# Optimization experiments

Hardware: AMD Instinct MI355X
Metric: run time of the kernel (lower is better)

Reference implementation:

```python
import jax, jax.numpy as jnp
import numpy as np

N_NODES = 100000
N_EDGES = 1250000
HID = 64
IN_CH = 64
OUT_CH = 16
N_GRAPHS = 512


def setup_inputs() -> dict:
    key = jax.random.key(0)
    ks = jax.random.split(key, 20)
    x = jax.random.normal(ks[0], (N_NODES, IN_CH), dtype=jnp.float32)
    edge_index = jax.random.randint(ks[1], (2, N_EDGES), 0, N_NODES, dtype=jnp.int64)
    batch = jnp.sort(jax.random.randint(ks[2], (N_NODES,), 0, N_GRAPHS, dtype=jnp.int64))
    s_in = 1.0 / np.sqrt(IN_CH)
    s_h = 1.0 / np.sqrt(HID)
    u = lambda k, shp, s: jax.random.uniform(k, shp, jnp.float32, -s, s)
    return {
        "x": x, "edge_index": edge_index, "batch": batch,
        "W0": u(ks[3], (IN_CH, HID), s_in), "b0": u(ks[4], (HID,), s_in),
        "W1a": u(ks[5], (HID, HID), s_h), "b1a": u(ks[6], (HID,), s_h),
        "W1b": u(ks[7], (HID, HID), s_h), "b1b": u(ks[8], (HID,), s_h),
        "W2a": u(ks[9], (HID, HID), s_h), "b2a": u(ks[10], (HID,), s_h),
        "W2b": u(ks[11], (HID, HID), s_h), "b2b": u(ks[12], (HID,), s_h),
        "W3a": u(ks[13], (HID, HID), s_h), "b3a": u(ks[14], (HID,), s_h),
        "W3b": u(ks[15], (HID, HID), s_h), "b3b": u(ks[16], (HID,), s_h),
        "Wl": u(ks[17], (HID, OUT_CH), s_h), "bl": u(ks[18], (OUT_CH,), s_h),
    }


def _gin_conv(h, src, dst, Wa, ba, Wb, bb):
    # GINConv, eps=0: mlp(x_i + sum_{j->i} x_j); mlp = Linear,ReLU,Linear
    agg = jax.ops.segment_sum(h[src], dst, num_segments=N_NODES)  # [N, HID]
    z = h + agg
    return jax.nn.relu(z @ Wa + ba) @ Wb + bb


def reference(x, edge_index, batch, W0, b0, W1a, b1a, W1b, b1b,
              W2a, b2a, W2b, b2b, W3a, b3a, W3b, b3b, Wl, bl):
    src, dst = edge_index[0], edge_index[1]
    h = jax.nn.relu(x @ W0 + b0)
    h = jax.nn.relu(_gin_conv(h, src, dst, W1a, b1a, W1b, b1b))
    h = jax.nn.relu(_gin_conv(h, src, dst, W2a, b2a, W2b, b2b))
    h = jax.nn.relu(_gin_conv(h, src, dst, W3a, b3a, W3b, b3b))
    # global mean pool over graphs
    sums = jax.ops.segment_sum(h, batch, num_segments=N_GRAPHS)  # [G, HID]
    cnts = jax.ops.segment_sum(jnp.ones((N_NODES,), h.dtype), batch, num_segments=N_GRAPHS)
    pooled = sums / jnp.maximum(cnts, 1.0)[:, None]
    # dropout p=0.5 is identity in eval mode
    return pooled @ Wl + bl  # [G, OUT_CH]
```

## Files before the change

kernel.cpp:

```cpp
#include <hip/hip_runtime.h>
#include <hip/hip_fp16.h>

#define N_NODES 100000
#define N_EDGES 1250000
#define HID 64
#define N_GRAPHS 512
#define OUT_CH 16

#define NSUP 196
#define SB_CAP 8192
#define E_BLK 2048
#define NPB ((N_EDGES + E_BLK - 1) / E_BLK)
#define TILE2 ((N_NODES + 127) / 128)
#define NWP 6
#define TSTRIDE 68
#define AGG_BLOCKS 3125
#define SMEM_UNION 37888

typedef _Float16 h16;
typedef _Float16 half2_t __attribute__((ext_vector_type(2)));
typedef _Float16 f16x8 __attribute__((ext_vector_type(8)));
typedef float f32x4 __attribute__((ext_vector_type(4)));

__device__ __forceinline__ void acc8(uint4 u, float* a) {
    half2_t h0 = __builtin_bit_cast(half2_t, u.x);
    half2_t h1 = __builtin_bit_cast(half2_t, u.y);
    half2_t h2 = __builtin_bit_cast(half2_t, u.z);
    half2_t h3 = __builtin_bit_cast(half2_t, u.w);
    a[0] += (float)h0[0]; a[1] += (float)h0[1];
    a[2] += (float)h1[0]; a[3] += (float)h1[1];
    a[4] += (float)h2[0]; a[5] += (float)h2[1];
    a[6] += (float)h3[0]; a[7] += (float)h3[1];
}

__device__ __forceinline__ unsigned pack2(float x, float y) {
    half2_t o;
    o[0] = (h16)x;
    o[1] = (h16)y;
    return __builtin_bit_cast(unsigned, o);
}

__global__ __launch_bounds__(256) void k_part(const int* __restrict__ src,
                                              const int* __restrict__ dst,
                                              int* __restrict__ cnt,
                                              int* __restrict__ buckets,
                                              const float* __restrict__ W1a,
                                              const float* __restrict__ W1b,
                                              const float* __restrict__ W2a,
                                              const float* __restrict__ W2b,
                                              const float* __restrict__ W3a,
                                              const float* __restrict__ W3b,
                                              h16* __restrict__ WF) {
    __shared__ int hist[256];
    __shared__ int gbase[256];
    __shared__ int tsum[256];
    __shared__ __align__(16) int stage[E_BLK];

    int b = blockIdx.x;
    int t = threadIdx.x;

    if (b < NPB) {
        int e0 = b * E_BLK;
        int eN = N_EDGES - e0;
        if (eN > E_BLK) eN = E_BLK;

        hist[t] = 0;
        __syncthreads();
        for (int i = t; i < eN; i += 256) atomicAdd(&hist[dst[e0 + i] >> 9], 1);
        __syncthreads();

        int c = hist[t];
        tsum[t] = c;
        __syncthreads();
        for (int off = 1; off < 256; off <<= 1) {
            int u = (t >= off) ? tsum[t - off] : 0;
            __syncthreads();
            tsum[t] += u;
            __syncthreads();
        }
        int pref = tsum[t] - c;
        if (t < NSUP && c > 0) gbase[t] = atomicAdd(&cnt[t], c);
        hist[t] = pref;
        __syncthreads();

        for (int i = t; i < eN; i += 256) {
            int s = src[e0 + i];
            int d = dst[e0 + i];
            int p = atomicAdd(&hist[d >> 9], 1);
            stage[p] = ((d & 511) << 17) | s;
        }
        __syncthreads();

        if (t < NSUP && c > 0) {
            int lstart = hist[t] - c;
            int gb = gbase[t];
            int cap = SB_CAP - gb;
            int n = c < cap ? c : (cap > 0 ? cap : 0);
            int* dp = buckets + (size_t)t * SB_CAP + gb;
            int r = 0;
            while (r < n && (((size_t)(dp + r)) & 15)) { dp[r] = stage[lstart + r]; ++r; }
            for (; r + 4 <= n; r += 4) {
                int4 v;
                v.x = stage[lstart + r];
                v.y = stage[lstart + r + 1];
                v.z = stage[lstart + r + 2];
                v.w = stage[lstart + r + 3];
                *(int4*)(dp + r) = v;
            }
            for (; r < n; ++r) dp[r] = stage[lstart + r];
        }
    } else {
        const float* Ws[NWP] = {W1a, W1b, W2a, W2b, W3a, W3b};
        const float* W = Ws[b - NPB];
        h16* dstW = WF + (size_t)(b - NPB) * 4096;
#pragma unroll
        for (int i = 0; i < 16; ++i) {
            int s = t + 256 * i;
            int k = s >> 6, col = s & 63;
            int kc = k >> 5, quad = (k >> 3) & 3, j = k & 7;
            int c = col >> 4, n = col & 15;
            dstW[((c * 2 + kc) * 4 + quad) * 128 + n * 8 + j] = (h16)W[s];
        }
    }
}

__global__ __launch_bounds__(256) void k_sortlin(const int* __restrict__ cnt,
                                                 int* __restrict__ buckets,
                                                 int* __restrict__ rowptrS,
                                                 const float* __restrict__ W0,
                                                 const float* __restrict__ B0,
                                                 const float* __restrict__ Xin,
                                                 h16* __restrict__ Hout) {
    __shared__ __align__(16) char smem[SMEM_UNION];
    int b = blockIdx.x;
    int t = threadIdx.x;

    if (b < NSUP) {
        int* srt  = (int*)smem;
        int* hist = (int*)(smem + 32768);
        int* curs = (int*)(smem + 34816);
        int* tsum = (int*)(smem + 36864);
        int s = b;
        int n = cnt[s];
        n = n < SB_CAP ? n : SB_CAP;
        int* gb = buckets + (size_t)s * SB_CAP;
        int sBase = s * SB_CAP;

        hist[t] = 0;
        hist[t + 256] = 0;
        __syncthreads();
        for (int i = t; i < n; i += 256) atomicAdd(&hist[gb[i] >> 17], 1);
        __syncthreads();

        int c0 = hist[2 * t], c1 = hist[2 * t + 1];
        int tot = c0 + c1;
        tsum[t] = tot;
        __syncthreads();
        for (int off = 1; off < 256; off <<= 1) {
            int u = (t >= off) ? tsum[t - off] : 0;
            __syncthreads();
            tsum[t] += u;
            __syncthreads();
        }
        int pref = tsum[t] - tot;
        curs[2 * t] = pref;
        curs[2 * t + 1] = pref + c0;
        rowptrS[s * 513 + 2 * t] = sBase + pref;
        rowptrS[s * 513 + 2 * t + 1] = sBase + pref + c0;
        if (t == 255) rowptrS[s * 513 + 512] = sBase + n;
        __syncthreads();

        for (int i = t; i < n; i += 256) {
            int rec = gb[i];
            int pos = atomicAdd(&curs[rec >> 17], 1);
            srt[pos] = rec;
        }
        __syncthreads();
        for (int i = t; i < n; i += 256) gb[i] = srt[i];
    } else {
        float* sT = (float*)smem;
        int lb = b - NSUP;
        int w = t >> 6, lane = t & 63;
        int n16 = lane & 15, quad = lane >> 4;
        float* T = sT + w * 16 * TSTRIDE;

        f16x8 bw[4][2];
#pragma unroll
        for (int c = 0; c < 4; ++c)
#pragma unroll
            for (int kc = 0; kc < 2; ++kc) {
                f16x8 v;
#pragma unroll
                for (int j = 0; j < 8; ++j)
                    v[j] = (h16)W0[(kc * 32 + quad * 8 + j) * 64 + c * 16 + n16];
                bw[c][kc] = v;
            }
        float bv[4];
#pragma unroll
        for (int c = 0; c < 4; ++c) bv[c] = B0[c * 16 + n16];

#pragma unroll
        for (int tt = 0; tt < 2; ++tt) {
            int rbase = lb * 128 + tt * 64 + w * 16;
            int arow = rbase + n16;
            int crow = arow < N_NODES ? arow : N_NODES - 1;
            f16x8 a[2];
#pragma unroll
            for (int kc = 0; kc < 2; ++kc) {
                const float4* xp = (const float4*)(Xin + (size_t)crow * HID + kc * 32 + quad * 8);
                float4 p = xp[0], q = xp[1];
                f16x8 v;
                v[0] = (h16)p.x; v[1] = (h16)p.y; v[2] = (h16)p.z; v[3] = (h16)p.w;
                v[4] = (h16)q.x; v[5] = (h16)q.y; v[6] = (h16)q.z; v[7] = (h16)q.w;
                a[kc] = v;
            }

            f32x4 acc[4];
#pragma unroll
            for (int c = 0; c < 4; ++c) {
                acc[c] = (f32x4){bv[c], bv[c], bv[c], bv[c]};
#pragma unroll
                for (int kc = 0; kc < 2; ++kc)
                    acc[c] = __builtin_amdgcn_mfma_f32_16x16x32_f16(a[kc], bw[c][kc], acc[c], 0, 0, 0);
            }

#pragma unroll
            for (int c = 0; c < 4; ++c)
#pragma unroll
                for (int r = 0; r < 4; ++r)
                    T[(quad * 4 + r) * TSTRIDE + c * 16 + n16] = fmaxf(acc[c][r], 0.f);
            {
                int rl = lane >> 2, seg = lane & 3;
                int row = rbase + rl;
                if (row < N_NODES) {
                    const float* tr = &T[rl * TSTRIDE + seg * 16];
                    f16x8 o0, o1;
#pragma unroll
                    for (int i = 0; i < 8; ++i) {
                        o0[i] = (h16)tr[i];
                        o1[i] = (h16)tr[8 + i];
                    }
                    f16x8* dp = (f16x8*)(Hout + (size_t)row * HID + seg * 16);
                    dp[0] = o0;
                    dp[1] = o1;
                }
            }
            __syncthreads();
        }
    }
}

__global__ __launch_bounds__(256) void k_aggregate(const int* __restrict__ rowptrS,
                                                   const int* __restrict__ buckets,
                                                   const h16* __restrict__ H,
                                                   h16* __restrict__ Z) {
    const uint4* H8 = (const uint4*)H;
    uint4* Z8 = (uint4*)Z;
    int lane = threadIdx.x & 63;
    int part = lane >> 3, sub = lane & 7;
    int gwave = (blockIdx.x * 256 + threadIdx.x) >> 6;
    int nw = (gridDim.x * 256) >> 6;
    for (int i0 = gwave * 8; i0 < N_NODES; i0 += nw * 8) {
        int i = i0 + part;
        bool valid = i < N_NODES;
        int iv = valid ? i : N_NODES - 1;
        int s = iv >> 9, l = iv & 511;
        int start = rowptrS[s * 513 + l];
        int end = valid ? rowptrS[s * 513 + l + 1] : start;
        float a[8] = {0.f, 0.f, 0.f, 0.f, 0.f, 0.f, 0.f, 0.f};
        acc8(H8[(size_t)iv * 8 + sub], a);
        int deg = end - start;
        if (deg > 0) {
            int last = end - 1;
            int ix[16];
#pragma unroll
            for (int k = 0; k < 16; ++k) {
                int p = start + k;
                ix[k] = buckets[p < last ? p : last] & 0x1FFFF;
            }
            uint4 u[8];
#pragma unroll
            for (int k = 0; k < 8; ++k)
                if (deg > k) u[k] = H8[(size_t)ix[k] * 8 + sub];
#pragma unroll
            for (int k = 0; k < 8; ++k)
                if (deg > k) acc8(u[k], a);
            if (deg > 8) {
#pragma unroll
                for (int k = 0; k < 8; ++k)
                    if (deg > 8 + k) u[k] = H8[(size_t)ix[8 + k] * 8 + sub];
#pragma unroll
                for (int k = 0; k < 8; ++k)
                    if (deg > 8 + k) acc8(u[k], a);
            }
            if (deg > 16) {
                int j = start + 16;
                for (; j + 8 <= end; j += 8) {
                    int s0 = buckets[j] & 0x1FFFF;
                    int s1 = buckets[j + 1] & 0x1FFFF;
                    int s2 = buckets[j + 2] & 0x1FFFF;
                    int s3 = buckets[j + 3] & 0x1FFFF;
                    int s4 = buckets[j + 4] & 0x1FFFF;
                    int s5 = buckets[j + 5] & 0x1FFFF;
                    int s6 = buckets[j + 6] & 0x1FFFF;
                    int s7 = buckets[j + 7] & 0x1FFFF;
                    uint4 v0 = H8[(size_t)s0 * 8 + sub];
                    uint4 v1 = H8[(size_t)s1 * 8 + sub];
                    uint4 v2 = H8[(size_t)s2 * 8 + sub];
                    uint4 v3 = H8[(size_t)s3 * 8 + sub];
                    uint4 v4 = H8[(size_t)s4 * 8 + sub];
                    uint4 v5 = H8[(size_t)s5 * 8 + sub];
                    uint4 v6 = H8[(size_t)s6 * 8 + sub];
                    uint4 v7 = H8[(size_t)s7 * 8 + sub];
                    acc8(v0, a); acc8(v1, a); acc8(v2, a); acc8(v3, a);
                    acc8(v4, a); acc8(v5, a); acc8(v6, a); acc8(v7, a);
                }
                if (j + 4 <= end) {
                    int s0 = buckets[j] & 0x1FFFF;
                    int s1 = buckets[j + 1] & 0x1FFFF;
                    int s2 = buckets[j + 2] & 0x1FFFF;
                    int s3 = buckets[j + 3] & 0x1FFFF;
                    uint4 v0 = H8[(size_t)s0 * 8 + sub];
                    uint4 v1 = H8[(size_t)s1 * 8 + sub];
                    uint4 v2 = H8[(size_t)s2 * 8 + sub];
                    uint4 v3 = H8[(size_t)s3 * 8 + sub];
                    acc8(v0, a); acc8(v1, a); acc8(v2, a); acc8(v3, a);
                    j += 4;
                }
                if (j + 2 <= end) {
                    int s0 = buckets[j] & 0x1FFFF;
                    int s1 = buckets[j + 1] & 0x1FFFF;
                    uint4 v0 = H8[(size_t)s0 * 8 + sub];
                    uint4 v1 = H8[(size_t)s1 * 8 + sub];
                    acc8(v0, a); acc8(v1, a);
                    j += 2;
                }
                if (j < end) {
                    int s0 = buckets[j] & 0x1FFFF;
                    acc8(H8[(size_t)s0 * 8 + sub], a);
                }
            }
        }
        if (valid) {
            uint4 o;
            o.x = pack2(a[0], a[1]);
            o.y = pack2(a[2], a[3]);
            o.z = pack2(a[4], a[5]);
            o.w = pack2(a[6], a[7]);
            Z8[(size_t)i * 8 + sub] = o;
        }
    }
}

__global__ __launch_bounds__(256) void k_mlp(const h16* __restrict__ WaF,
                                             const float* __restrict__ Ba,
                                             const h16* __restrict__ WbF,
                                             const float* __restrict__ Bb,
                                             const h16* __restrict__ Zin,
                                             h16* __restrict__ Hout) {
    __shared__ __align__(16) float sT[4 * 16 * TSTRIDE];
    int t = threadIdx.x;
    int w = t >> 6, lane = t & 63;
    int n16 = lane & 15, quad = lane >> 4;
    float* T = sT + w * 16 * TSTRIDE;

    f16x8 bwa[4][2], bwb[4][2];
#pragma unroll
    for (int c = 0; c < 4; ++c)
#pragma unroll
        for (int kc = 0; kc < 2; ++kc) {
            int f = ((c * 2 + kc) * 4 + quad) * 128 + n16 * 8;
            bwa[c][kc] = *(const f16x8*)(WaF + f);
            bwb[c][kc] = *(const f16x8*)(WbF + f);
        }
    float bva[4], bvb[4];
#pragma unroll
    for (int c = 0; c < 4; ++c) {
        bva[c] = Ba[c * 16 + n16];
        bvb[c] = Bb[c * 16 + n16];
    }

#pragma unroll
    for (int tt = 0; tt < 2; ++tt) {
        int rbase = blockIdx.x * 128 + tt * 64 + w * 16;
        int arow = rbase + n16;
        int crow = arow < N_NODES ? arow : N_NODES - 1;
        const f16x8* zp = (const f16x8*)(Zin + (size_t)crow * HID + quad * 8);
        f16x8 a0 = zp[0];
        f16x8 a1 = zp[4];

        f32x4 acc[4];
#pragma unroll
        for (int c = 0; c < 4; ++c) {
            acc[c] = (f32x4){bva[c], bva[c], bva[c], bva[c]};
            acc[c] = __builtin_amdgcn_mfma_f32_16x16x32_f16(a0, bwa[c][0], acc[c], 0, 0, 0);
            acc[c] = __builtin_amdgcn_mfma_f32_16x16x32_f16(a1, bwa[c][1], acc[c], 0, 0, 0);
        }

#pragma unroll
        for (int c = 0; c < 4; ++c)
#pragma unroll
            for (int r = 0; r < 4; ++r)
                T[(quad * 4 + r) * TSTRIDE + c * 16 + n16] = fmaxf(acc[c][r], 0.f);

        f16x8 ta[2];
#pragma unroll
        for (int kc = 0; kc < 2; ++kc) {
            float4 p = *(const float4*)&T[n16 * TSTRIDE + kc * 32 + quad * 8];
            float4 q = *(const float4*)&T[n16 * TSTRIDE + kc * 32 + quad * 8 + 4];
            f16x8 v;
            v[0] = (h16)p.x; v[1] = (h16)p.y; v[2] = (h16)p.z; v[3] = (h16)p.w;
            v[4] = (h16)q.x; v[5] = (h16)q.y; v[6] = (h16)q.z; v[7] = (h16)q.w;
            ta[kc] = v;
        }

#pragma unroll
        for (int c = 0; c < 4; ++c) {
            acc[c] = (f32x4){bvb[c], bvb[c], bvb[c], bvb[c]};
            acc[c] = __builtin_amdgcn_mfma_f32_16x16x32_f16(ta[0], bwb[c][0], acc[c], 0, 0, 0);
            acc[c] = __builtin_amdgcn_mfma_f32_16x16x32_f16(ta[1], bwb[c][1], acc[c], 0, 0, 0);
        }

#pragma unroll
        for (int c = 0; c < 4; ++c)
#pragma unroll
            for (int r = 0; r < 4; ++r)
                T[(quad * 4 + r) * TSTRIDE + c * 16 + n16] = fmaxf(acc[c][r], 0.f);
        {
            int rl = lane >> 2, seg = lane & 3;
            int row = rbase + rl;
            if (row < N_NODES) {
                const float* tr = &T[rl * TSTRIDE + seg * 16];
                f16x8 o0, o1;
#pragma unroll
                for (int i = 0; i < 8; ++i) {
                    o0[i] = (h16)tr[i];
                    o1[i] = (h16)tr[8 + i];
                }
                f16x8* dp = (f16x8*)(Hout + (size_t)row * HID + seg * 16);
                dp[0] = o0;
                dp[1] = o1;
            }
        }
    }
}

__global__ __launch_bounds__(256) void k_poolfinal(const h16* __restrict__ H,
                                                   const int* __restrict__ batch,
                                                   const float* __restrict__ Wl,
                                                   const float* __restrict__ bl,
                                                   float* __restrict__ out) {
    __shared__ float sp[4 * HID];
    int g = blockIdx.x;
    int t = threadIdx.x;
    int lane = t & 63, w = t >> 6;
    int lo = 0, hi = N_NODES;
    while (lo < hi) { int m = (lo + hi) >> 1; if (batch[m] < g) lo = m + 1; else hi = m; }
    int start = lo;
    hi = N_NODES;
    while (lo < hi) { int m = (lo + hi) >> 1; if (batch[m] < g + 1) lo = m + 1; else hi = m; }
    int end = lo;
    float s0 = 0.f, s1 = 0.f, s2 = 0.f, s3 = 0.f;
    int r = start + w;
    for (; r + 12 < end; r += 16) {
        float v0 = (float)H[(size_t)r * HID + lane];
        float v1 = (float)H[(size_t)(r + 4) * HID + lane];
        float v2 = (float)H[(size_t)(r + 8) * HID + lane];
        float v3 = (float)H[(size_t)(r + 12) * HID + lane];
        s0 += v0; s1 += v1; s2 += v2; s3 += v3;
    }
    for (; r < end; r += 4) s0 += (float)H[(size_t)r * HID + lane];
    sp[w * HID + lane] = s0 + s1 + s2 + s3;
    __syncthreads();
    if (t < HID) {
        float tot = sp[t] + sp[HID + t] + sp[2 * HID + t] + sp[3 * HID + t];
        float c = (end > start) ? (float)(end - start) : 1.0f;
        sp[t] = tot / c;
    }
    __syncthreads();
    if (t < OUT_CH) {
        float acc = bl[t];
#pragma unroll
        for (int k = 0; k < HID; ++k) acc += sp[k] * Wl[k * OUT_CH + t];
        out[g * OUT_CH + t] = acc;
    }
}

extern "C" void kernel_launch(void* const* d_in, const int* in_sizes, int n_in,
                              void* d_out, int out_size, void* d_ws, size_t ws_size,
                              hipStream_t stream) {
    const float* x     = (const float*)d_in[0];
    const int*   edge  = (const int*)d_in[1];
    const int*   batch = (const int*)d_in[2];
    const float* W0  = (const float*)d_in[3];
    const float* b0  = (const float*)d_in[4];
    const float* W1a = (const float*)d_in[5];
    const float* b1a = (const float*)d_in[6];
    const float* W1b = (const float*)d_in[7];
    const float* b1b = (const float*)d_in[8];
    const float* W2a = (const float*)d_in[9];
    const float* b2a = (const float*)d_in[10];
    const float* W2b = (const float*)d_in[11];
    const float* b2b = (const float*)d_in[12];
    const float* W3a = (const float*)d_in[13];
    const float* b3a = (const float*)d_in[14];
    const float* W3b = (const float*)d_in[15];
    const float* b3b = (const float*)d_in[16];
    const float* Wl  = (const float*)d_in[17];
    const float* bl  = (const float*)d_in[18];
    float* out = (float*)d_out;

    const int* src = edge;
    const int* dst = edge + N_EDGES;

    h16* HA = (h16*)d_ws;
    h16* Z  = HA + (size_t)N_NODES * HID;
    int* cnt     = (int*)(Z + (size_t)N_NODES * HID);
    int* rowptrS = cnt + NSUP;
    int* buckets = rowptrS + NSUP * 513;
    h16* WF      = (h16*)(buckets + (size_t)NSUP * SB_CAP);
    h16* W1aF = WF;
    h16* W1bF = WF + 4096 * 1;
    h16* W2aF = WF + 4096 * 2;
    h16* W2bF = WF + 4096 * 3;
    h16* W3aF = WF + 4096 * 4;
    h16* W3bF = WF + 4096 * 5;

    hipMemsetAsync(cnt, 0, NSUP * sizeof(int), stream);
    k_part<<<NPB + NWP, 256, 0, stream>>>(src, dst, cnt, buckets,
        W1a, W1b, W2a, W2b, W3a, W3b, WF);
    k_sortlin<<<NSUP + TILE2, 256, 0, stream>>>(cnt, buckets, rowptrS, W0, b0, x, HA);

    k_aggregate<<<AGG_BLOCKS, 256, 0, stream>>>(rowptrS, buckets, HA, Z);
    k_mlp<<<TILE2, 256, 0, stream>>>(W1aF, b1a, W1bF, b1b, Z, HA);

    k_aggregate<<<AGG_BLOCKS, 256, 0, stream>>>(rowptrS, buckets, HA, Z);
    k_mlp<<<TILE2, 256, 0, stream>>>(W2aF, b2a, W2bF, b2b, Z, HA);

    k_aggregate<<<AGG_BLOCKS, 256, 0, stream>>>(rowptrS, buckets, HA, Z);
    k_mlp<<<TILE2, 256, 0, stream>>>(W3aF, b3a, W3bF, b3b, Z, HA);

    k_poolfinal<<<N_GRAPHS, 256, 0, stream>>>(HA, batch, Wl, bl, out);
}
```

Before: 274.8 us.

## Fuse final MLP with mean-pool accumulation and simplify aggregate gather loop

The last GIN MLP now accumulates its ReLU output directly into per-graph sums, using shared-memory slots plus global atomics, so the final H is never written or re-read. A small kernel then divides by the node counts and applies the output linear layer. The aggregate kernel's gather loop drops the prefetched 16-index front end and uses one plain unrolled-by-8 loop, which shrinks code and register use but may lose some early memory-level parallelism for low-degree nodes. The workspace layout is rearranged and the memset is widened to also zero the graph sums.

```diff
diff --git a/kernel.cpp b/kernel.cpp
--- a/kernel.cpp
+++ b/kernel.cpp
@@ -16,6 +16,7 @@
 #define TSTRIDE 68
 #define AGG_BLOCKS 3125
 #define SMEM_UNION 37888
+#define GP_SLOTS 16
 
 typedef _Float16 h16;
 typedef _Float16 half2_t __attribute__((ext_vector_type(2)));
@@ -269,77 +270,50 @@
         int end = valid ? rowptrS[s * 513 + l + 1] : start;
         float a[8] = {0.f, 0.f, 0.f, 0.f, 0.f, 0.f, 0.f, 0.f};
         acc8(H8[(size_t)iv * 8 + sub], a);
-        int deg = end - start;
-        if (deg > 0) {
-            int last = end - 1;
-            int ix[16];
-#pragma unroll
-            for (int k = 0; k < 16; ++k) {
-                int p = start + k;
-                ix[k] = buckets[p < last ? p : last] & 0x1FFFF;
-            }
-            uint4 u[8];
-#pragma unroll
-            for (int k = 0; k < 8; ++k)
-                if (deg > k) u[k] = H8[(size_t)ix[k] * 8 + sub];
-#pragma unroll
-            for (int k = 0; k < 8; ++k)
-                if (deg > k) acc8(u[k], a);
-            if (deg > 8) {
-#pragma unroll
-                for (int k = 0; k < 8; ++k)
-                    if (deg > 8 + k) u[k] = H8[(size_t)ix[8 + k] * 8 + sub];
-#pragma unroll
-                for (int k = 0; k < 8; ++k)
-                    if (deg > 8 + k) acc8(u[k], a);
-            }
-            if (deg > 16) {
-                int j = start + 16;
-                for (; j + 8 <= end; j += 8) {
-                    int s0 = buckets[j] & 0x1FFFF;
-                    int s1 = buckets[j + 1] & 0x1FFFF;
-                    int s2 = buckets[j + 2] & 0x1FFFF;
-                    int s3 = buckets[j + 3] & 0x1FFFF;
-                    int s4 = buckets[j + 4] & 0x1FFFF;
-                    int s5 = buckets[j + 5] & 0x1FFFF;
-                    int s6 = buckets[j + 6] & 0x1FFFF;
-                    int s7 = buckets[j + 7] & 0x1FFFF;
-                    uint4 v0 = H8[(size_t)s0 * 8 + sub];
-                    uint4 v1 = H8[(size_t)s1 * 8 + sub];
-                    uint4 v2 = H8[(size_t)s2 * 8 + sub];
-                    uint4 v3 = H8[(size_t)s3 * 8 + sub];
-                    uint4 v4 = H8[(size_t)s4 * 8 + sub];
-                    uint4 v5 = H8[(size_t)s5 * 8 + sub];
-                    uint4 v6 = H8[(size_t)s6 * 8 + sub];
-                    uint4 v7 = H8[(size_t)s7 * 8 + sub];
-                    acc8(v0, a); acc8(v1, a); acc8(v2, a); acc8(v3, a);
-                    acc8(v4, a); acc8(v5, a); acc8(v6, a); acc8(v7, a);
-                }
-                if (j + 4 <= end) {
-                    int s0 = buckets[j] & 0x1FFFF;
-                    int s1 = buckets[j + 1] & 0x1FFFF;
-                    int s2 = buckets[j + 2] & 0x1FFFF;
-                    int s3 = buckets[j + 3] & 0x1FFFF;
-                    uint4 v0 = H8[(size_t)s0 * 8 + sub];
-                    uint4 v1 = H8[(size_t)s1 * 8 + sub];
-                    uint4 v2 = H8[(size_t)s2 * 8 + sub];
-                    uint4 v3 = H8[(size_t)s3 * 8 + sub];
-                    acc8(v0, a); acc8(v1, a); acc8(v2, a); acc8(v3, a);
-                    j += 4;
-                }
-                if (j + 2 <= end) {
-                    int s0 = buckets[j] & 0x1FFFF;
-                    int s1 = buckets[j + 1] & 0x1FFFF;
-                    uint4 v0 = H8[(size_t)s0 * 8 + sub];
-                    uint4 v1 = H8[(size_t)s1 * 8 + sub];
-                    acc8(v0, a); acc8(v1, a);
-                    j += 2;
-                }
-                if (j < end) {
-                    int s0 = buckets[j] & 0x1FFFF;
-                    acc8(H8[(size_t)s0 * 8 + sub], a);
-                }
-            }
+        int j = start;
+        for (; j + 8 <= end; j += 8) {
+            int s0 = buckets[j] & 0x1FFFF;
+            int s1 = buckets[j + 1] & 0x1FFFF;
+            int s2 = buckets[j + 2] & 0x1FFFF;
+            int s3 = buckets[j + 3] & 0x1FFFF;
+            int s4 = buckets[j + 4] & 0x1FFFF;
+            int s5 = buckets[j + 5] & 0x1FFFF;
+            int s6 = buckets[j + 6] & 0x1FFFF;
+            int s7 = buckets[j + 7] & 0x1FFFF;
+            uint4 u0 = H8[(size_t)s0 * 8 + sub];
+            uint4 u1 = H8[(size_t)s1 * 8 + sub];
+            uint4 u2 = H8[(size_t)s2 * 8 + sub];
+            uint4 u3 = H8[(size_t)s3 * 8 + sub];
+            uint4 u4 = H8[(size_t)s4 * 8 + sub];
+            uint4 u5 = H8[(size_t)s5 * 8 + sub];
+            uint4 u6 = H8[(size_t)s6 * 8 + sub];
+            uint4 u7 = H8[(size_t)s7 * 8 + sub];
+            acc8(u0, a); acc8(u1, a); acc8(u2, a); acc8(u3, a);
+            acc8(u4, a); acc8(u5, a); acc8(u6, a); acc8(u7, a);
+        }
+        if (j + 4 <= end) {
+            int s0 = buckets[j] & 0x1FFFF;
+            int s1 = buckets[j + 1] & 0x1FFFF;
+            int s2 = buckets[j + 2] & 0x1FFFF;
+            int s3 = buckets[j + 3] & 0x1FFFF;
+            uint4 u0 = H8[(size_t)s0 * 8 + sub];
+            uint4 u1 = H8[(size_t)s1 * 8 + sub];
+            uint4 u2 = H8[(size_t)s2 * 8 + sub];
+            uint4 u3 = H8[(size_t)s3 * 8 + sub];
+            acc8(u0, a); acc8(u1, a); acc8(u2, a); acc8(u3, a);
+            j += 4;
+        }
+        if (j + 2 <= end) {
+            int s0 = buckets[j] & 0x1FFFF;
+            int s1 = buckets[j + 1] & 0x1FFFF;
+            uint4 u0 = H8[(size_t)s0 * 8 + sub];
+            uint4 u1 = H8[(size_t)s1 * 8 + sub];
+            acc8(u0, a); acc8(u1, a);
+            j += 2;
+        }
+        if (j < end) {
+            int s0 = buckets[j] & 0x1FFFF;
+            acc8(H8[(size_t)s0 * 8 + sub], a);
         }
         if (valid) {
             uint4 o;
@@ -445,38 +419,134 @@
     }
 }
 
-__global__ __launch_bounds__(256) void k_poolfinal(const h16* __restrict__ H,
-                                                   const int* __restrict__ batch,
-                                                   const float* __restrict__ Wl,
-                                                   const float* __restrict__ bl,
-                                                   float* __restrict__ out) {
-    __shared__ float sp[4 * HID];
+__global__ __launch_bounds__(256) void k_mlppool(const h16* __restrict__ WaF,
+                                                 const float* __restrict__ Ba,
+                                                 const h16* __restrict__ WbF,
+                                                 const float* __restrict__ Bb,
+                                                 const h16* __restrict__ Zin,
+                                                 const int* __restrict__ batch,
+                                                 float* __restrict__ gsum) {
+    __shared__ __align__(16) float sT[4 * 16 * TSTRIDE];
+    __shared__ float gpart[GP_SLOTS * HID];
+    int t = threadIdx.x;
+    int w = t >> 6, lane = t & 63;
+    int n16 = lane & 15, quad = lane >> 4;
+    float* T = sT + w * 16 * TSTRIDE;
+
+    int row0 = blockIdx.x * 128;
+    int rowN = row0 + 127; if (rowN >= N_NODES) rowN = N_NODES - 1;
+    int gmin = batch[row0];
+    for (int idx = t; idx < GP_SLOTS * HID; idx += 256) gpart[idx] = 0.f;
+
+    f16x8 bwa[4][2], bwb[4][2];
+#pragma unroll
+    for (int c = 0; c < 4; ++c)
+#pragma unroll
+        for (int kc = 0; kc < 2; ++kc) {
+            int f = ((c * 2 + kc) * 4 + quad) * 128 + n16 * 8;
+            bwa[c][kc] = *(const f16x8*)(WaF + f);
+            bwb[c][kc] = *(const f16x8*)(WbF + f);
+        }
+    float bva[4], bvb[4];
+#pragma unroll
+    for (int c = 0; c < 4; ++c) {
+        bva[c] = Ba[c * 16 + n16];
+        bvb[c] = Bb[c * 16 + n16];
+    }
+    __syncthreads();
+
+#pragma unroll
+    for (int tt = 0; tt < 2; ++tt) {
+        int rbase = blockIdx.x * 128 + tt * 64 + w * 16;
+        int arow = rbase + n16;
+        int crow = arow < N_NODES ? arow : N_NODES - 1;
+        const f16x8* zp = (const f16x8*)(Zin + (size_t)crow * HID + quad * 8);
+        f16x8 a0 = zp[0];
+        f16x8 a1 = zp[4];
+
+        f32x4 acc[4];
+#pragma unroll
+        for (int c = 0; c < 4; ++c) {
+            acc[c] = (f32x4){bva[c], bva[c], bva[c], bva[c]};
+            acc[c] = __builtin_amdgcn_mfma_f32_16x16x32_f16(a0, bwa[c][0], acc[c], 0, 0, 0);
+            acc[c] = __builtin_amdgcn_mfma_f32_16x16x32_f16(a1, bwa[c][1], acc[c], 0, 0, 0);
+        }
+
+#pragma unroll
+        for (int c = 0; c < 4; ++c)
+#pragma unroll
+            for (int r = 0; r < 4; ++r)
+                T[(quad * 4 + r) * TSTRIDE + c * 16 + n16] = fmaxf(acc[c][r], 0.f);
+
+        f16x8 ta[2];
+#pragma unroll
+        for (int kc = 0; kc < 2; ++kc) {
+            float4 p = *(const float4*)&T[n16 * TSTRIDE + kc * 32 + quad * 8];
+            float4 q = *(const float4*)&T[n16 * TSTRIDE + kc * 32 + quad * 8 + 4];
+            f16x8 v;
+            v[0] = (h16)p.x; v[1] = (h16)p.y; v[2] = (h16)p.z; v[3] = (h16)p.w;
+            v[4] = (h16)q.x; v[5] = (h16)q.y; v[6] = (h16)q.z; v[7] = (h16)q.w;
+            ta[kc] = v;
+        }
+
+#pragma unroll
+        for (int c = 0; c < 4; ++c) {
+            acc[c] = (f32x4){bvb[c], bvb[c], bvb[c], bvb[c]};
+            acc[c] = __builtin_amdgcn_mfma_f32_16x16x32_f16(ta[0], bwb[c][0], acc[c], 0, 0, 0);
+            acc[c] = __builtin_amdgcn_mfma_f32_16x16x32_f16(ta[1], bwb[c][1], acc[c], 0, 0, 0);
+        }
+
+#pragma unroll
+        for (int c = 0; c < 4; ++c)
+#pragma unroll
+            for (int r = 0; r < 4; ++r)
+                T[(quad * 4 + r) * TSTRIDE + c * 16 + n16] = fmaxf(acc[c][r], 0.f);
+        {
+            int rl = lane >> 2, seg = lane & 3;
+            int row = rbase + rl;
+            if (row < N_NODES) {
+                const float* tr = &T[rl * TSTRIDE + seg * 16];
+                int g = batch[row];
+                int slot = g - gmin;
+                if (slot < GP_SLOTS) {
+#pragma unroll
+                    for (int k2 = 0; k2 < 16; ++k2)
+                        atomicAdd(&gpart[slot * HID + seg * 16 + k2], tr[k2]);
+                } else {
+#pragma unroll
+                    for (int k2 = 0; k2 < 16; ++k2)
+                        atomicAdd(&gsum[(size_t)g * HID + seg * 16 + k2], tr[k2]);
+                }
+            }
+        }
+    }
+    __syncthreads();
+    int gmax = batch[rowN];
+    int span = gmax - gmin + 1;
+    if (span > GP_SLOTS) span = GP_SLOTS;
+    for (int idx = t; idx < span * HID; idx += 256) {
+        float v = gpart[idx];
+        if (v != 0.f)
+            atomicAdd(&gsum[((size_t)gmin + (idx >> 6)) * HID + (idx & 63)], v);
+    }
+}
+
+__global__ __launch_bounds__(64) void k_final(const float* __restrict__ gsum,
+                                              const int* __restrict__ batch,
+                                              const float* __restrict__ Wl,
+                                              const float* __restrict__ bl,
+                                              float* __restrict__ out) {
+    __shared__ float sp[HID];
     int g = blockIdx.x;
     int t = threadIdx.x;
-    int lane = t & 63, w = t >> 6;
     int lo = 0, hi = N_NODES;
     while (lo < hi) { int m = (lo + hi) >> 1; if (batch[m] < g) lo = m + 1; else hi = m; }
     int start = lo;
     hi = N_NODES;
     while (lo < hi) { int m = (lo + hi) >> 1; if (batch[m] < g + 1) lo = m + 1; else hi = m; }
     int end = lo;
-    float s0 = 0.f, s1 = 0.f, s2 = 0.f, s3 = 0.f;
-    int r = start + w;
-    for (; r + 12 < end; r += 16) {
-        float v0 = (float)H[(size_t)r * HID + lane];
-        float v1 = (float)H[(size_t)(r + 4) * HID + lane];
-        float v2 = (float)H[(size_t)(r + 8) * HID + lane];
-        float v3 = (float)H[(size_t)(r + 12) * HID + lane];
-        s0 += v0; s1 += v1; s2 += v2; s3 += v3;
-    }
-    for (; r < end; r += 4) s0 += (float)H[(size_t)r * HID + lane];
-    sp[w * HID + lane] = s0 + s1 + s2 + s3;
-    __syncthreads();
-    if (t < HID) {
-        float tot = sp[t] + sp[HID + t] + sp[2 * HID + t] + sp[3 * HID + t];
-        float c = (end > start) ? (float)(end - start) : 1.0f;
-        sp[t] = tot / c;
-    }
+    float c = (end > start) ? (float)(end - start) : 1.0f;
+    sp[t] = gsum[(size_t)g * HID + t] / c;
     __syncthreads();
     if (t < OUT_CH) {
         float acc = bl[t];
@@ -513,12 +583,13 @@
     const int* src = edge;
     const int* dst = edge + N_EDGES;
 
-    h16* HA = (h16*)d_ws;
-    h16* Z  = HA + (size_t)N_NODES * HID;
-    int* cnt     = (int*)(Z + (size_t)N_NODES * HID);
+    float* gsum  = (float*)d_ws;
+    int* cnt     = (int*)(gsum + N_GRAPHS * HID);
     int* rowptrS = cnt + NSUP;
     int* buckets = rowptrS + NSUP * 513;
     h16* WF      = (h16*)(buckets + (size_t)NSUP * SB_CAP);
+    h16* HA      = WF + 4096 * NWP;
+    h16* Z       = HA + (size_t)N_NODES * HID;
     h16* W1aF = WF;
     h16* W1bF = WF + 4096 * 1;
     h16* W2aF = WF + 4096 * 2;
@@ -526,7 +597,7 @@
     h16* W3aF = WF + 4096 * 4;
     h16* W3bF = WF + 4096 * 5;
 
-    hipMemsetAsync(cnt, 0, NSUP * sizeof(int), stream);
+    hipMemsetAsync(gsum, 0, N_GRAPHS * HID * sizeof(float) + NSUP * sizeof(int), stream);
     k_part<<<NPB + NWP, 256, 0, stream>>>(src, dst, cnt, buckets,
         W1a, W1b, W2a, W2b, W3a, W3b, WF);
     k_sortlin<<<NSUP + TILE2, 256, 0, stream>>>(cnt, buckets, rowptrS, W0, b0, x, HA);
@@ -538,7 +609,7 @@
     k_mlp<<<TILE2, 256, 0, stream>>>(W2aF, b2a, W2bF, b2b, Z, HA);
 
     k_aggregate<<<AGG_BLOCKS, 256, 0, stream>>>(rowptrS, buckets, HA, Z);
-    k_mlp<<<TILE2, 256, 0, stream>>>(W3aF, b3a, W3bF, b3b, Z, HA);
-
-    k_poolfinal<<<N_GRAPHS, 256, 0, stream>>>(HA, batch, Wl, bl, out);
-}
+    k_mlppool<<<TILE2, 256, 0, stream>>>(W3aF, b3a, W3bF, b3b, Z, batch, gsum);
+
+    k_final<<<N_GRAPHS, 64, 0, stream>>>(gsum, batch, Wl, bl, out);
+}
```

Measured after the change: 341.6 us. 1.24x slower.

## Split node range and overlap second-half aggregation with first-half MLP

Applied to the files above, without the earlier changes.

Each GIN layer is split at a node boundary. The first half is aggregated, then a combined kernel aggregates the second half while other blocks run the MLP on the first half, and a final MLP pass covers the second half. Ping-pong H buffers (HA/HB) are added so the MLP output never overwrites inputs that concurrent aggregation blocks still read. The aggregate kernel also drops its special 16-neighbour prefetch path in favour of a plain unrolled-by-8 loop. This adds an extra launch per layer and mixes heterogeneous work inside one grid.

```diff
diff --git a/kernel.cpp b/kernel.cpp
--- a/kernel.cpp
+++ b/kernel.cpp
@@ -14,8 +14,13 @@
 #define TILE2 ((N_NODES + 127) / 128)
 #define NWP 6
 #define TSTRIDE 68
-#define AGG_BLOCKS 3125
 #define SMEM_UNION 37888
+
+#define SPLIT 49920
+#define AGA_BLKS (SPLIT / 32)
+#define AGB_BLKS ((N_NODES - SPLIT + 31) / 32)
+#define MLPA_BLKS (SPLIT / 128)
+#define MLPB_BLKS ((N_NODES - SPLIT + 127) / 128)
 
 typedef _Float16 h16;
 typedef _Float16 half2_t __attribute__((ext_vector_type(2)));
@@ -38,6 +43,164 @@
     o[0] = (h16)x;
     o[1] = (h16)y;
     return __builtin_bit_cast(unsigned, o);
+}
+
+__device__ __forceinline__ void agg8rows(const int* __restrict__ rowptrS,
+                                         const int* __restrict__ buckets,
+                                         const uint4* __restrict__ H8,
+                                         uint4* __restrict__ Z8,
+                                         int i0, int rhi, int part, int sub) {
+    int i = i0 + part;
+    bool valid = i < rhi;
+    int iv = valid ? i : rhi - 1;
+    int s = iv >> 9, l = iv & 511;
+    int start = rowptrS[s * 513 + l];
+    int end = valid ? rowptrS[s * 513 + l + 1] : start;
+    float a[8] = {0.f, 0.f, 0.f, 0.f, 0.f, 0.f, 0.f, 0.f};
+    acc8(H8[(size_t)iv * 8 + sub], a);
+    int j = start;
+    for (; j + 8 <= end; j += 8) {
+        int s0 = buckets[j] & 0x1FFFF;
+        int s1 = buckets[j + 1] & 0x1FFFF;
+        int s2 = buckets[j + 2] & 0x1FFFF;
+        int s3 = buckets[j + 3] & 0x1FFFF;
+        int s4 = buckets[j + 4] & 0x1FFFF;
+        int s5 = buckets[j + 5] & 0x1FFFF;
+        int s6 = buckets[j + 6] & 0x1FFFF;
+        int s7 = buckets[j + 7] & 0x1FFFF;
+        uint4 u0 = H8[(size_t)s0 * 8 + sub];
+        uint4 u1 = H8[(size_t)s1 * 8 + sub];
+        uint4 u2 = H8[(size_t)s2 * 8 + sub];
+        uint4 u3 = H8[(size_t)s3 * 8 + sub];
+        uint4 u4 = H8[(size_t)s4 * 8 + sub];
+        uint4 u5 = H8[(size_t)s5 * 8 + sub];
+        uint4 u6 = H8[(size_t)s6 * 8 + sub];
+        uint4 u7 = H8[(size_t)s7 * 8 + sub];
+        acc8(u0, a); acc8(u1, a); acc8(u2, a); acc8(u3, a);
+        acc8(u4, a); acc8(u5, a); acc8(u6, a); acc8(u7, a);
+    }
+    if (j + 4 <= end) {
+        int s0 = buckets[j] & 0x1FFFF;
+        int s1 = buckets[j + 1] & 0x1FFFF;
+        int s2 = buckets[j + 2] & 0x1FFFF;
+        int s3 = buckets[j + 3] & 0x1FFFF;
+        uint4 u0 = H8[(size_t)s0 * 8 + sub];
+        uint4 u1 = H8[(size_t)s1 * 8 + sub];
+        uint4 u2 = H8[(size_t)s2 * 8 + sub];
+        uint4 u3 = H8[(size_t)s3 * 8 + sub];
+        acc8(u0, a); acc8(u1, a); acc8(u2, a); acc8(u3, a);
+        j += 4;
+    }
+    if (j + 2 <= end) {
+        int s0 = buckets[j] & 0x1FFFF;
+        int s1 = buckets[j + 1] & 0x1FFFF;
+        uint4 u0 = H8[(size_t)s0 * 8 + sub];
+        uint4 u1 = H8[(size_t)s1 * 8 + sub];
+        acc8(u0, a); acc8(u1, a);
+        j += 2;
+    }
+    if (j < end) {
+        int s0 = buckets[j] & 0x1FFFF;
+        acc8(H8[(size_t)s0 * 8 + sub], a);
+    }
+    if (valid) {
+        uint4 o;
+        o.x = pack2(a[0], a[1]);
+        o.y = pack2(a[2], a[3]);
+        o.z = pack2(a[4], a[5]);
+        o.w = pack2(a[6], a[7]);
+        Z8[(size_t)i * 8 + sub] = o;
+    }
+}
+
+__device__ __forceinline__ void mlp_tile128(const h16* __restrict__ WaF,
+                                            const float* __restrict__ Ba,
+                                            const h16* __restrict__ WbF,
+                                            const float* __restrict__ Bb,
+                                            const h16* __restrict__ Zin,
+                                            h16* __restrict__ Hout,
+                                            int row0, float* T, int w, int lane) {
+    int n16 = lane & 15, quad = lane >> 4;
+
+    f16x8 bwa[4][2], bwb[4][2];
+#pragma unroll
+    for (int c = 0; c < 4; ++c)
+#pragma unroll
+        for (int kc = 0; kc < 2; ++kc) {
+            int f = ((c * 2 + kc) * 4 + quad) * 128 + n16 * 8;
+            bwa[c][kc] = *(const f16x8*)(WaF + f);
+            bwb[c][kc] = *(const f16x8*)(WbF + f);
+        }
+    float bva[4], bvb[4];
+#pragma unroll
+    for (int c = 0; c < 4; ++c) {
+        bva[c] = Ba[c * 16 + n16];
+        bvb[c] = Bb[c * 16 + n16];
+    }
+
+#pragma unroll
+    for (int tt = 0; tt < 2; ++tt) {
+        int rbase = row0 + tt * 64 + w * 16;
+        int arow = rbase + n16;
+        int crow = arow < N_NODES ? arow : N_NODES - 1;
+        const f16x8* zp = (const f16x8*)(Zin + (size_t)crow * HID + quad * 8);
+        f16x8 a0 = zp[0];
+        f16x8 a1 = zp[4];
+
+        f32x4 acc[4];
+#pragma unroll
+        for (int c = 0; c < 4; ++c) {
+            acc[c] = (f32x4){bva[c], bva[c], bva[c], bva[c]};
+            acc[c] = __builtin_amdgcn_mfma_f32_16x16x32_f16(a0, bwa[c][0], acc[c], 0, 0, 0);
+            acc[c] = __builtin_amdgcn_mfma_f32_16x16x32_f16(a1, bwa[c][1], acc[c], 0, 0, 0);
+        }
+
+#pragma unroll
+        for (int c = 0; c < 4; ++c)
+#pragma unroll
+            for (int r = 0; r < 4; ++r)
+                T[(quad * 4 + r) * TSTRIDE + c * 16 + n16] = fmaxf(acc[c][r], 0.f);
+
+        f16x8 ta[2];
+#pragma unroll
+        for (int kc = 0; kc < 2; ++kc) {
+            float4 p = *(const float4*)&T[n16 * TSTRIDE + kc * 32 + quad * 8];
+            float4 q = *(const float4*)&T[n16 * TSTRIDE + kc * 32 + quad * 8 + 4];
+            f16x8 v;
+            v[0] = (h16)p.x; v[1] = (h16)p.y; v[2] = (h16)p.z; v[3] = (h16)p.w;
+            v[4] = (h16)q.x; v[5] = (h16)q.y; v[6] = (h16)q.z; v[7] = (h16)q.w;
+            ta[kc] = v;
+        }
+
+#pragma unroll
+        for (int c = 0; c < 4; ++c) {
+            acc[c] = (f32x4){bvb[c], bvb[c], bvb[c], bvb[c]};
+            acc[c] = __builtin_amdgcn_mfma_f32_16x16x32_f16(ta[0], bwb[c][0], acc[c], 0, 0, 0);
+            acc[c] = __builtin_amdgcn_mfma_f32_16x16x32_f16(ta[1], bwb[c][1], acc[c], 0, 0, 0);
+        }
+
+#pragma unroll
+        for (int c = 0; c < 4; ++c)
+#pragma unroll
+            for (int r = 0; r < 4; ++r)
+                T[(quad * 4 + r) * TSTRIDE + c * 16 + n16] = fmaxf(acc[c][r], 0.f);
+        {
+            int rl = lane >> 2, seg = lane & 3;
+            int row = rbase + rl;
+            if (row < N_NODES) {
+                const float* tr = &T[rl * TSTRIDE + seg * 16];
+                f16x8 o0, o1;
+#pragma unroll
+                for (int i = 0; i < 8; ++i) {
+                    o0[i] = (h16)tr[i];
+                    o1[i] = (h16)tr[8 + i];
+                }
+                f16x8* dp = (f16x8*)(Hout + (size_t)row * HID + seg * 16);
+                dp[0] = o0;
+                dp[1] = o1;
+            }
+        }
+    }
 }
 
 __global__ __launch_bounds__(256) void k_part(const int* __restrict__ src,
@@ -253,102 +416,43 @@
 __global__ __launch_bounds__(256) void k_aggregate(const int* __restrict__ rowptrS,
                                                    const int* __restrict__ buckets,
                                                    const h16* __restrict__ H,
-                                                   h16* __restrict__ Z) {
+                                                   h16* __restrict__ Z,
+                                                   int rlo, int rhi) {
     const uint4* H8 = (const uint4*)H;
     uint4* Z8 = (uint4*)Z;
     int lane = threadIdx.x & 63;
     int part = lane >> 3, sub = lane & 7;
     int gwave = (blockIdx.x * 256 + threadIdx.x) >> 6;
     int nw = (gridDim.x * 256) >> 6;
-    for (int i0 = gwave * 8; i0 < N_NODES; i0 += nw * 8) {
-        int i = i0 + part;
-        bool valid = i < N_NODES;
-        int iv = valid ? i : N_NODES - 1;
-        int s = iv >> 9, l = iv & 511;
-        int start = rowptrS[s * 513 + l];
-        int end = valid ? rowptrS[s * 513 + l + 1] : start;
-        float a[8] = {0.f, 0.f, 0.f, 0.f, 0.f, 0.f, 0.f, 0.f};
-        acc8(H8[(size_t)iv * 8 + sub], a);
-        int deg = end - start;
-        if (deg > 0) {
-            int last = end - 1;
-            int ix[16];
-#pragma unroll
-            for (int k = 0; k < 16; ++k) {
-                int p = start + k;
-                ix[k] = buckets[p < last ? p : last] & 0x1FFFF;
-            }
-            uint4 u[8];
-#pragma unroll
-            for (int k = 0; k < 8; ++k)
-                if (deg > k) u[k] = H8[(size_t)ix[k] * 8 + sub];
-#pragma unroll
-            for (int k = 0; k < 8; ++k)
-                if (deg > k) acc8(u[k], a);
-            if (deg > 8) {
-#pragma unroll
-                for (int k = 0; k < 8; ++k)
-                    if (deg > 8 + k) u[k] = H8[(size_t)ix[8 + k] * 8 + sub];
-#pragma unroll
-                for (int k = 0; k < 8; ++k)
-                    if (deg > 8 + k) acc8(u[k], a);
-            }
-            if (deg > 16) {
-                int j = start + 16;
-                for (; j + 8 <= end; j += 8) {
-                    int s0 = buckets[j] & 0x1FFFF;
-                    int s1 = buckets[j + 1] & 0x1FFFF;
-                    int s2 = buckets[j + 2] & 0x1FFFF;
-                    int s3 = buckets[j + 3] & 0x1FFFF;
-                    int s4 = buckets[j + 4] & 0x1FFFF;
-                    int s5 = buckets[j + 5] & 0x1FFFF;
-                    int s6 = buckets[j + 6] & 0x1FFFF;
-                    int s7 = buckets[j + 7] & 0x1FFFF;
-                    uint4 v0 = H8[(size_t)s0 * 8 + sub];
-                    uint4 v1 = H8[(size_t)s1 * 8 + sub];
-                    uint4 v2 = H8[(size_t)s2 * 8 + sub];
-                    uint4 v3 = H8[(size_t)s3 * 8 + sub];
-                    uint4 v4 = H8[(size_t)s4 * 8 + sub];
-                    uint4 v5 = H8[(size_t)s5 * 8 + sub];
-                    uint4 v6 = H8[(size_t)s6 * 8 + sub];
-                    uint4 v7 = H8[(size_t)s7 * 8 + sub];
-                    acc8(v0, a); acc8(v1, a); acc8(v2, a); acc8(v3, a);
-                    acc8(v4, a); acc8(v5, a); acc8(v6, a); acc8(v7, a);
-                }
-                if (j + 4 <= end) {
-                    int s0 = buckets[j] & 0x1FFFF;
-                    int s1 = buckets[j + 1] & 0x1FFFF;
-                    int s2 = buckets[j + 2] & 0x1FFFF;
-                    int s3 = buckets[j + 3] & 0x1FFFF;
-                    uint4 v0 = H8[(size_t)s0 * 8 + sub];
-                    uint4 v1 = H8[(size_t)s1 * 8 + sub];
-                    uint4 v2 = H8[(size_t)s2 * 8 + sub];
-                    uint4 v3 = H8[(size_t)s3 * 8 + sub];
-                    acc8(v0, a); acc8(v1, a); acc8(v2, a); acc8(v3, a);
-                    j += 4;
-                }
-                if (j + 2 <= end) {
-                    int s0 = buckets[j] & 0x1FFFF;
-                    int s1 = buckets[j + 1] & 0x1FFFF;
-                    uint4 v0 = H8[(size_t)s0 * 8 + sub];
-                    uint4 v1 = H8[(size_t)s1 * 8 + sub];
-                    acc8(v0, a); acc8(v1, a);
-                    j += 2;
-                }
-                if (j < end) {
-                    int s0 = buckets[j] & 0x1FFFF;
-                    acc8(H8[(size_t)s0 * 8 + sub], a);
-                }
-            }
-        }
-        if (valid) {
-            uint4 o;
-            o.x = pack2(a[0], a[1]);
-            o.y = pack2(a[2], a[3]);
-            o.z = pack2(a[4], a[5]);
-            o.w = pack2(a[6], a[7]);
-            Z8[(size_t)i * 8 + sub] = o;
-        }
+    for (int i0 = rlo + gwave * 8; i0 < rhi; i0 += nw * 8)
+        agg8rows(rowptrS, buckets, H8, Z8, i0, rhi, part, sub);
+}
+
+__global__ __launch_bounds__(256) void k_aggmlp2(const int* __restrict__ rowptrS,
+                                                 const int* __restrict__ buckets,
+                                                 const h16* __restrict__ Hin,
+                                                 h16* __restrict__ Z,
+                                                 const h16* __restrict__ WaF,
+                                                 const float* __restrict__ Ba,
+                                                 const h16* __restrict__ WbF,
+                                                 const float* __restrict__ Bb,
+                                                 h16* __restrict__ Hout) {
+    __shared__ __align__(16) float sT[4 * 16 * TSTRIDE];
+    int b = blockIdx.x;
+    int t = threadIdx.x;
+    if (b < AGB_BLKS) {
+        const uint4* H8 = (const uint4*)Hin;
+        uint4* Z8 = (uint4*)Z;
+        int lane = t & 63;
+        int part = lane >> 3, sub = lane & 7;
+        int gwave = (b * 256 + t) >> 6;
+        int nw = (AGB_BLKS * 256) >> 6;
+        for (int i0 = SPLIT + gwave * 8; i0 < N_NODES; i0 += nw * 8)
+            agg8rows(rowptrS, buckets, H8, Z8, i0, N_NODES, part, sub);
+    } else {
+        int lb = b - AGB_BLKS;
+        int w = t >> 6, lane = t & 63;
+        mlp_tile128(WaF, Ba, WbF, Bb, Z, Hout, lb * 128, sT + w * 16 * TSTRIDE, w, lane);
     }
 }
 
@@ -357,92 +461,13 @@
                                              const h16* __restrict__ WbF,
                                              const float* __restrict__ Bb,
                                              const h16* __restrict__ Zin,
-                                             h16* __restrict__ Hout) {
+                                             h16* __restrict__ Hout,
+                                             int base) {
     __shared__ __align__(16) float sT[4 * 16 * TSTRIDE];
     int t = threadIdx.x;
     int w = t >> 6, lane = t & 63;
-    int n16 = lane & 15, quad = lane >> 4;
-    float* T = sT + w * 16 * TSTRIDE;
-
-    f16x8 bwa[4][2], bwb[4][2];
-#pragma unroll
-    for (int c = 0; c < 4; ++c)
-#pragma unroll
-        for (int kc = 0; kc < 2; ++kc) {
-            int f = ((c * 2 + kc) * 4 + quad) * 128 + n16 * 8;
-            bwa[c][kc] = *(const f16x8*)(WaF + f);
-            bwb[c][kc] = *(const f16x8*)(WbF + f);
-        }
-    float bva[4], bvb[4];
-#pragma unroll
-    for (int c = 0; c < 4; ++c) {
-        bva[c] = Ba[c * 16 + n16];
-        bvb[c] = Bb[c * 16 + n16];
-    }
-
-#pragma unroll
-    for (int tt = 0; tt < 2; ++tt) {
-        int rbase = blockIdx.x * 128 + tt * 64 + w * 16;
-        int arow = rbase + n16;
-        int crow = arow < N_NODES ? arow : N_NODES - 1;
-        const f16x8* zp = (const f16x8*)(Zin + (size_t)crow * HID + quad * 8);
-        f16x8 a0 = zp[0];
-        f16x8 a1 = zp[4];
-
-        f32x4 acc[4];
-#pragma unroll
-        for (int c = 0; c < 4; ++c) {
-            acc[c] = (f32x4){bva[c], bva[c], bva[c], bva[c]};
-            acc[c] = __builtin_amdgcn_mfma_f32_16x16x32_f16(a0, bwa[c][0], acc[c], 0, 0, 0);
-            acc[c] = __builtin_amdgcn_mfma_f32_16x16x32_f16(a1, bwa[c][1], acc[c], 0, 0, 0);
-        }
-
-#pragma unroll
-        for (int c = 0; c < 4; ++c)
-#pragma unroll
-            for (int r = 0; r < 4; ++r)
-                T[(quad * 4 + r) * TSTRIDE + c * 16 + n16] = fmaxf(acc[c][r], 0.f);
-
-        f16x8 ta[2];
-#pragma unroll
-        for (int kc = 0; kc < 2; ++kc) {
-            float4 p = *(const float4*)&T[n16 * TSTRIDE + kc * 32 + quad * 8];
-            float4 q = *(const float4*)&T[n16 * TSTRIDE + kc * 32 + quad * 8 + 4];
-            f16x8 v;
-            v[0] = (h16)p.x; v[1] = (h16)p.y; v[2] = (h16)p.z; v[3] = (h16)p.w;
-            v[4] = (h16)q.x; v[5] = (h16)q.y; v[6] = (h16)q.z; v[7] = (h16)q.w;
-            ta[kc] = v;
-        }
-
-#pragma unroll
-        for (int c = 0; c < 4; ++c) {
-            acc[c] = (f32x4){bvb[c], bvb[c], bvb[c], bvb[c]};
-            acc[c] = __builtin_amdgcn_mfma_f32_16x16x32_f16(ta[0], bwb[c][0], acc[c], 0, 0, 0);
-            acc[c] = __builtin_amdgcn_mfma_f32_16x16x32_f16(ta[1], bwb[c][1], acc[c], 0, 0, 0);
-        }
-
-#pragma unroll
-        for (int c = 0; c < 4; ++c)
-#pragma unroll
-            for (int r = 0; r < 4; ++r)
-                T[(quad * 4 + r) * TSTRIDE + c * 16 + n16] = fmaxf(acc[c][r], 0.f);
-        {
-            int rl = lane >> 2, seg = lane & 3;
-            int row = rbase + rl;
-            if (row < N_NODES) {
-                const float* tr = &T[rl * TSTRIDE + seg * 16];
-                f16x8 o0, o1;
-#pragma unroll
-                for (int i = 0; i < 8; ++i) {
-                    o0[i] = (h16)tr[i];
-                    o1[i] = (h16)tr[8 + i];
-                }
-                f16x8* dp = (f16x8*)(Hout + (size_t)row * HID + seg * 16);
-                dp[0] = o0;
-                dp[1] = o1;
-            }
-        }
-    }
+    mlp_tile128(WaF, Ba, WbF, Bb, Zin, Hout, base + blockIdx.x * 128,
+                sT + w * 16 * TSTRIDE, w, lane);
 }
 
 __global__ __launch_bounds__(256) void k_poolfinal(const h16* __restrict__ H,
@@ -514,7 +539,8 @@
     const int* dst = edge + N_EDGES;
 
     h16* HA = (h16*)d_ws;
-    h16* Z  = HA + (size_t)N_NODES * HID;
+    h16* HB = HA + (size_t)N_NODES * HID;
+    h16* Z  = HB + (size_t)N_NODES * HID;
     int* cnt     = (int*)(Z + (size_t)N_NODES * HID);
     int* rowptrS = cnt + NSUP;
     int* buckets = rowptrS + NSUP * 513;
@@ -531,14 +557,20 @@
         W1a, W1b, W2a, W2b, W3a, W3b, WF);
     k_sortlin<<<NSUP + TILE2, 256, 0, stream>>>(cnt, buckets, rowptrS, W0, b0, x, HA);
 
-    k_aggregate<<<AGG_BLOCKS, 256, 0, stream>>>(rowptrS, buckets, HA, Z);
-    k_mlp<<<TILE2, 256, 0, stream>>>(W1aF, b1a, W1bF, b1b, Z, HA);
-
-    k_aggregate<<<AGG_BLOCKS, 256, 0, stream>>>(rowptrS, buckets, HA, Z);
-    k_mlp<<<TILE2, 256, 0, stream>>>(W2aF, b2a, W2bF, b2b, Z, HA);
-
-    k_aggregate<<<AGG_BLOCKS, 256, 0, stream>>>(rowptrS, buckets, HA, Z);
-    k_mlp<<<TILE2, 256, 0, stream>>>(W3aF, b3a, W3bF, b3b, Z, HA);
-
-    k_poolfinal<<<N_GRAPHS, 256, 0, stream>>>(HA, batch, Wl, bl, out);
-}
+    k_aggregate<<<AGA_BLKS, 256, 0, stream>>>(rowptrS, buckets, HA, Z, 0, SPLIT);
+    k_aggmlp2<<<AGB_BLKS + MLPA_BLKS, 256, 0, stream>>>(rowptrS, buckets, HA, Z,
+        W1aF, b1a, W1bF, b1b, HB);
+    k_mlp<<<MLPB_BLKS, 256, 0, stream>>>(W1aF, b1a, W1bF, b1b, Z, HB, SPLIT);
+
+    k_aggregate<<<AGA_BLKS, 256, 0, stream>>>(rowptrS, buckets, HB, Z, 0, SPLIT);
+    k_aggmlp2<<<AGB_BLKS + MLPA_BLKS, 256, 0, stream>>>(rowptrS, buckets, HB, Z,
+        W2aF, b2a, W2bF, b2b, HA);
+    k_mlp<<<MLPB_BLKS, 256, 0, stream>>>(W2aF, b2a, W2bF, b2b, Z, HA, SPLIT);
+
+    k_aggregate<<<AGA_BLKS, 256, 0, stream>>>(rowptrS, buckets, HA, Z, 0, SPLIT);
+    k_aggmlp2<<<AGB_BLKS + MLPA_BLKS, 256, 0, stream>>>(rowptrS, buckets, HA, Z,
+        W3aF, b3a, W3bF, b3b, HB);
+    k_mlp<<<MLPB_BLKS, 256, 0, stream>>>(W3aF, b3a, W3bF, b3b, Z, HB, SPLIT);
+
+    k_poolfinal<<<N_GRAPHS, 256, 0, stream>>>(HB, batch, Wl, bl, out);
+}
```

New measurement: 282.9 us. 3.0% more time.
